# Kernel tuning notes

Measured on AMD Instinct MI355X. Metric: run time of the kernel, lower is better.

The kernel has to match this reference:

```python
import jax, jax.numpy as jnp
import numpy as np

TEMPERATURE = 0.1
MAX_POS = 6
MAX_NEG = 30
POS_NEG_RATIO = 1.0
NEG_K = max(6, MAX_NEG)  # static top-k width for negatives


def setup_inputs() -> dict:
    key = jax.random.key(0)
    k1, k2 = jax.random.split(key)
    K, D = 8192, 256
    features = jax.random.normal(k1, (K, D), dtype=jnp.float32)
    labels = jax.random.randint(k2, (K,), 0, 64, dtype=jnp.int64)
    return {"features": features, "labels": labels}


def reference(features, labels):
    K = features.shape[0]
    # L2-normalize embeddings (F.normalize, dim=1)
    f = features / jnp.clip(jnp.linalg.norm(features, axis=1, keepdims=True), 1e-12)
    sim = jnp.matmul(f, f.T) / TEMPERATURE                      # [K, K]
    sim = sim - jax.lax.stop_gradient(jnp.max(sim, axis=1, keepdims=True))
    exp_sim = jnp.exp(sim)

    eye = jnp.eye(K, dtype=bool)
    same = labels[:, None] == labels[None, :]
    mask_pos = same & ~eye                                      # same label, off-diagonal
    mask_neg = ~same                                            # 1 - mask_pos - eye

    n_pos = jnp.sum(mask_pos, axis=1).astype(jnp.int32)         # [K]
    n_neg = jnp.sum(mask_neg, axis=1).astype(jnp.int32)         # [K]

    # per-anchor dynamic sample counts (vectorized version of the python loop)
    max_pos_i = jnp.minimum(
        n_pos,
        jnp.maximum(1, jnp.minimum(MAX_POS, (n_neg.astype(jnp.float32) * POS_NEG_RATIO).astype(jnp.int32))),
    )
    max_neg_i = jnp.minimum(n_neg, NEG_K)
    valid_row = (n_pos > 0) & (n_neg > 0)
    max_pos_i = jnp.where(valid_row, max_pos_i, 0)
    max_neg_i = jnp.where(valid_row, max_neg_i, 0)

    rows = jnp.arange(K)[:, None]
    neg_inf = jnp.finfo(sim.dtype).min

    # top-k hard positives by similarity, masked to the first max_pos_i ranks
    pos_scores = jnp.where(mask_pos, sim, neg_inf)
    _, pos_idx = jax.lax.top_k(pos_scores, MAX_POS)             # [K, MAX_POS]
    pos_keep = (jnp.arange(MAX_POS)[None, :] < max_pos_i[:, None]).astype(sim.dtype)
    new_mask_pos = jnp.zeros((K, K), sim.dtype).at[rows, pos_idx].add(pos_keep)

    # random negatives: randperm emulated by top-k of uniform scores over neg slots
    rand = jax.random.uniform(jax.random.key(42), (K, K), dtype=jnp.float32)
    neg_scores = jnp.where(mask_neg, rand, -1.0)
    _, neg_idx = jax.lax.top_k(neg_scores, NEG_K)               # [K, NEG_K]
    neg_keep = (jnp.arange(NEG_K)[None, :] < max_neg_i[:, None]).astype(sim.dtype)
    new_mask_neg = jnp.zeros((K, K), sim.dtype).at[rows, neg_idx].add(neg_keep)

    numerator = jnp.sum(exp_sim * new_mask_pos, axis=1)
    denominator = jnp.sum(exp_sim * (new_mask_pos + new_mask_neg), axis=1)
    loss = -jnp.log(jnp.clip(numerator / denominator, 1e-8))
    return jnp.mean(loss)
```

## Files before the change

kernel.cpp:

```cpp
#include <hip/hip_runtime.h>
#include <hip/hip_fp16.h>
#include <math.h>
#include <stdint.h>


#define NEGK 30
#define MAXP 6
#define MAXBC 320
#define RGB 32

typedef _Float16 h2v __attribute__((ext_vector_type(2)));

__device__ __forceinline__ uint64_t mix64(uint64_t z) {
  z += 0x9E3779B97F4A7C15ULL;
  z = (z ^ (z >> 30)) * 0xBF58476D1CE4E5B9ULL;
  z = (z ^ (z >> 27)) * 0x94D049BB133111EBULL;
  return z ^ (z >> 31);
}

__device__ __forceinline__ float wave_reduce_add(float p) {
#pragma unroll
  for (int o = 32; o; o >>= 1) p += __shfl_down(p, o, 64);
  return p;
}

__device__ __forceinline__ float dot8h(uint4 a, uint4 b, float acc) {
  const h2v* pa = (const h2v*)&a;
  const h2v* pb = (const h2v*)&b;
#if __has_builtin(__builtin_amdgcn_fdot2)
#pragma unroll
  for (int q = 0; q < 4; ++q) acc = __builtin_amdgcn_fdot2(pa[q], pb[q], acc, false);
#else
#pragma unroll
  for (int q = 0; q < 4; ++q)
    acc += (float)pa[q].x * (float)pb[q].x + (float)pa[q].y * (float)pb[q].y;
#endif
  return acc;
}

__global__ __launch_bounds__(256) void k_prep(const float* __restrict__ F,
                                              const int* __restrict__ labels, int K,
                                              __half* __restrict__ Fh,
                                              int* __restrict__ g_start,
                                              int* __restrict__ g_soff,
                                              int* __restrict__ g_bucket,
                                              int4* __restrict__ g_meta) {
  __shared__ int cnt[64], start[65], cur[64], soff_s[64];
  const int tid = threadIdx.x;

  if ((int)blockIdx.x < K / 4) {
    const int row = blockIdx.x * 4 + (tid >> 6);
    const int lane = tid & 63;
    const float4 a = ((const float4*)(F + (size_t)row * 256))[lane];
    float p = a.x * a.x + a.y * a.y + a.z * a.z + a.w * a.w;
    p = wave_reduce_add(p);
    p = __shfl(p, 0, 64);
    const float inv = 1.0f / fmaxf(sqrtf(p), 1e-12f);
    union { __half2 h[2]; uint2 u; } cv;
    cv.h[0] = __float22half2_rn(make_float2(a.x * inv, a.y * inv));
    cv.h[1] = __float22half2_rn(make_float2(a.z * inv, a.w * inv));
    ((uint2*)(Fh + (size_t)row * 256))[lane] = cv.u;
    return;
  }

  if (tid < 64) cnt[tid] = 0;
  __syncthreads();
  for (int t = tid; t < K; t += 256) atomicAdd(&cnt[labels[t] & 63], 1);
  __syncthreads();
  if (tid == 0) {
    int acc = 0, sacc = 0;
    for (int l = 0; l < 64; ++l) {
      start[l] = acc;
      const int B = cnt[l];
      acc += B;
      soff_s[l] = sacc;
      const int Bc = B < MAXBC ? B : MAXBC;
      sacc += Bc * Bc;
    }
    start[64] = acc;
  }
  __syncthreads();
  if (tid < 64) { cur[tid] = start[tid]; g_soff[tid] = soff_s[tid]; }
  if (tid < 65) g_start[tid] = start[tid];
  __syncthreads();
  for (int t = tid; t < K; t += 256) {
    const int l = labels[t] & 63;
    const int p = atomicAdd(&cur[l], 1);
    g_bucket[p] = t;
    g_meta[t] = make_int4(start[l], cnt[l], p - start[l], soff_s[l]);
  }
}

template <int NCS>
__device__ __forceinline__ void gram_body(const __half* __restrict__ Fh,
                                          const int* __restrict__ g_bucket,
                                          const uint4* __restrict__ sw,
                                          float* __restrict__ outb,
                                          int bs, int Bc, int r0w, int lane) {
  const uint4* cp[NCS];
  int cq[NCS];
#pragma unroll
  for (int cs = 0; cs < NCS; ++cs) {
    const int cc = cs * 64 + lane;
    const bool valid = (cc < Bc);
    const int gq = g_bucket[bs + (valid ? cc : 0)];
    cq[cs] = valid ? cc : -1;
    cp[cs] = (const uint4*)(Fh + (size_t)gq * 256);
  }

  float acc[8][NCS];
#pragma unroll
  for (int r = 0; r < 8; ++r)
#pragma unroll
    for (int cs = 0; cs < NCS; ++cs) acc[r][cs] = 0.0f;

  for (int k = 0; k < 32; k += 2) {
    uint4 c0[NCS], c1[NCS];
#pragma unroll
    for (int cs = 0; cs < NCS; ++cs) { c0[cs] = cp[cs][k]; c1[cs] = cp[cs][k + 1]; }
#pragma unroll
    for (int r = 0; r < 8; ++r) {
      const uint4 a0 = sw[r * 32 + k];
      const uint4 a1 = sw[r * 32 + k + 1];
#pragma unroll
      for (int cs = 0; cs < NCS; ++cs) {
        acc[r][cs] = dot8h(c0[cs], a0, acc[r][cs]);
        acc[r][cs] = dot8h(c1[cs], a1, acc[r][cs]);
      }
    }
  }

#pragma unroll
  for (int r = 0; r < 8; ++r) {
    const int rr = r0w + r;
    if (rr < Bc) {
#pragma unroll
      for (int cs = 0; cs < NCS; ++cs) {
        const int cc = cq[cs];
        if (cc >= 0)
          outb[(size_t)rr * Bc + cc] = (rr == cc) ? -3.0e38f : acc[r][cs] * 10.0f;
      }
    }
  }
}

__global__ __launch_bounds__(256) void k_gram(const __half* __restrict__ Fh,
                                              const int* __restrict__ g_start,
                                              const int* __restrict__ g_soff,
                                              const int* __restrict__ g_bucket,
                                              float* __restrict__ g_sims) {
  __shared__ uint4 sA[RGB * 32];

  const int b  = blockIdx.x;
  const int bs = g_start[b];
  const int B  = g_start[b + 1] - bs;
  const int Bc = B < MAXBC ? B : MAXBC;
  const int r0 = blockIdx.y * RGB;
  if (r0 >= Bc) return;
  const int tid = threadIdx.x;

  for (int u = tid; u < RGB * 32; u += 256) {
    const int r = u >> 5, c = u & 31;
    const int rr = r0 + r;
    const int gr = g_bucket[bs + (rr < Bc ? rr : 0)];
    sA[u] = ((const uint4*)(Fh + (size_t)gr * 256))[c];
  }
  __syncthreads();

  const int wv = tid >> 6, lane = tid & 63;
  const uint4* sw = sA + (wv * 8) * 32;
  float* outb = g_sims + g_soff[b];
  const int r0w = r0 + wv * 8;

  if (Bc <= 128)
    gram_body<2>(Fh, g_bucket, sw, outb, bs, Bc, r0w, lane);
  else
    gram_body<5>(Fh, g_bucket, sw, outb, bs, Bc, r0w, lane);
}

__global__ __launch_bounds__(256) void k_anchor(
    const __half* __restrict__ Fh, const int* __restrict__ g_bucket,
    const int4* __restrict__ g_meta, const float* __restrict__ g_sims,
    float* __restrict__ g_part, int K) {
  __shared__ uint4 sA[4 * 32];
  const int wv = threadIdx.x >> 6;
  const int lane = threadIdx.x & 63;
  const int i = blockIdx.x * 4 + wv;

  ((uint2*)sA)[wv * 64 + lane] = ((const uint2*)(Fh + (size_t)i * 256))[lane];
  const uint4* sw = sA + wv * 32;

  const int4 mt = g_meta[i];
  const int bs = mt.x, B = mt.y;
  const int Bc = B < MAXBC ? B : MAXBC;
  int loc = mt.z;
  if (loc >= Bc) loc = 0;
  const int n_pos = B - 1;
  const int n_neg = K - B;
  const float* simrow = g_sims + mt.w + (size_t)loc * Bc;

  float v[5];
#pragma unroll
  for (int rr = 0; rr < 5; ++rr) {
    const int t = lane + rr * 64;
    v[rr] = (t < Bc) ? simrow[t] : -3.4e38f;
  }

  int t6 = n_neg < MAXP ? n_neg : MAXP;
  if (t6 < 1) t6 = 1;
  int take = n_pos < t6 ? n_pos : t6;
  if (n_pos <= 0 || n_neg <= 0) take = 0;
  const int target = (take > 0) ? (n_neg < NEGK ? n_neg : NEGK) : 0;

  const int s = lane & 3, g = lane >> 2;
  const int n0 = g, n1 = 16 + g;
  const uint64_t z0 = mix64(((uint64_t)(uint32_t)i << 32) | (uint32_t)n0);
  const uint64_t z1 = mix64(((uint64_t)(uint32_t)i << 32) | (uint32_t)n1);
  const unsigned int r0 = (unsigned int)(((uint64_t)(uint32_t)z0 * (uint64_t)n_neg) >> 32);
  const unsigned int r1 = (unsigned int)(((uint64_t)(uint32_t)z1 * (uint64_t)n_neg) >> 32);
  const int pos0 = (r0 < (unsigned int)bs) ? (int)r0 : (int)r0 + B;
  const int pos1 = (r1 < (unsigned int)bs) ? (int)r1 : (int)r1 + B;
  const bool pv0 = (n0 < target), pv1 = (n1 < target);
  const int j0 = pv0 ? g_bucket[pos0] : 0;
  const int j1 = pv1 ? g_bucket[pos1] : 0;
  const uint4* f0 = (const uint4*)(Fh + (size_t)j0 * 256);
  const uint4* f1 = (const uint4*)(Fh + (size_t)j1 * 256);
  float d0 = 0.0f, d1 = 0.0f;
#pragma unroll
  for (int k = 0; k < 8; ++k) {
    const uint4 aw = sw[k * 4 + s];
    d0 = dot8h(f0[k * 4 + s], aw, d0);
    d1 = dot8h(f1[k * 4 + s], aw, d1);
  }
  d0 += __shfl_xor(d0, 1, 64); d0 += __shfl_xor(d0, 2, 64);
  d1 += __shfl_xor(d1, 1, 64); d1 += __shfl_xor(d1, 2, 64);
  float e = 0.0f;
  if (s == 0) {
    if (pv0) e += expf(d0 * 10.0f);
    if (pv1) e += expf(d1 * 10.0f);
  }
  const float wsum = wave_reduce_add(e);

  float num = 0.0f;
  for (int r = 0; r < take; ++r) {
    float best = v[0];
#pragma unroll
    for (int c = 1; c < 5; ++c) best = fmaxf(best, v[c]);
#pragma unroll
    for (int o = 1; o < 64; o <<= 1) best = fmaxf(best, __shfl_xor(best, o, 64));
    num += expf(best);
#pragma unroll
    for (int c = 0; c < 5; ++c)
      if (v[c] == best) v[c] = -3.4e38f;
  }

  if (lane == 0) {
    float ls = 0.0f;
    if (take > 0) {
      const float denom = num + wsum;
      float ratio = denom > 0.0f ? num / denom : 0.0f;
      ratio = fmaxf(ratio, 1e-8f);
      ls = -logf(ratio);
    }
    g_part[i] = ls;
  }
}

__global__ __launch_bounds__(1024) void k_final(const float* __restrict__ g_part,
                                                float* __restrict__ out, int K) {
  __shared__ float s[16];
  float p = 0.0f;
  for (int t = threadIdx.x; t < K; t += 1024) p += g_part[t];
  p = wave_reduce_add(p);
  if ((threadIdx.x & 63) == 0) s[threadIdx.x >> 6] = p;
  __syncthreads();
  if (threadIdx.x == 0) {
    float tot = 0.0f;
#pragma unroll
    for (int w = 0; w < 16; ++w) tot += s[w];
    out[0] = tot / (float)K;
  }
}

extern "C" void kernel_launch(void* const* d_in, const int* in_sizes, int n_in,
                              void* d_out, int out_size, void* d_ws, size_t ws_size,
                              hipStream_t stream) {
  (void)n_in; (void)out_size; (void)ws_size;
  const float* F = (const float*)d_in[0];
  const int* labels = (const int*)d_in[1];
  const int K = in_sizes[1];
  float* out = (float*)d_out;

  char* ws = (char*)d_ws;
  size_t off = 0;
  int*   g_start  = (int*)(ws + off);   off += 512;
  int*   g_soff   = (int*)(ws + off);   off += 256;
  int*   g_bucket = (int*)(ws + off);   off += (size_t)K * 4;
  float* g_part   = (float*)(ws + off); off += (size_t)K * 4;
  off = (off + 255) & ~(size_t)255;
  int4*  g_meta   = (int4*)(ws + off);  off += (size_t)K * 16;
  __half* Fh      = (__half*)(ws + off); off += (size_t)K * 256 * 2;
  float* g_sims   = (float*)(ws + off);  off += (size_t)MAXBC * K * 4;

  k_prep<<<K / 4 + 1, 256, 0, stream>>>(F, labels, K, Fh, g_start, g_soff,
                                        g_bucket, g_meta);
  {
    dim3 grid(64, (MAXBC + RGB - 1) / RGB, 1);
    k_gram<<<grid, 256, 0, stream>>>(Fh, g_start, g_soff, g_bucket, g_sims);
  }
  k_anchor<<<K / 4, 256, 0, stream>>>(Fh, g_bucket, g_meta, g_sims, g_part, K);
  k_final<<<1, 1024, 0, stream>>>(g_part, out, K);
}
```

Measured before the change: 127.8 us.

## Split gram kernel columns across a third grid dimension of 64-wide tiles

The per-label gram kernel now launches a 3D grid and gives each block one 64-column tile, instead of having each wave loop over up to 5 column slices. This raises the number of blocks and cuts per-thread accumulator registers from 8xNCS to 8, which should improve occupancy and load balance across buckets. In exchange the shared row tile is reloaded once per column tile, and many blocks exit immediately when the bucket is small. Out-of-range row and column indices are now clamped to Bc-1 instead of 0.

New measurement: 114.5 us. -10.4%, faster.

```diff
diff --git a/kernel.cpp b/kernel.cpp
--- a/kernel.cpp
+++ b/kernel.cpp
@@ -8,6 +8,7 @@
 #define MAXP 6
 #define MAXBC 320
 #define RGB 32
+#define CGB 64
 
 typedef _Float16 h2v __attribute__((ext_vector_type(2)));
 
@@ -91,59 +92,6 @@
   }
 }
 
-template <int NCS>
-__device__ __forceinline__ void gram_body(const __half* __restrict__ Fh,
-                                          const int* __restrict__ g_bucket,
-                                          const uint4* __restrict__ sw,
-                                          float* __restrict__ outb,
-                                          int bs, int Bc, int r0w, int lane) {
-  const uint4* cp[NCS];
-  int cq[NCS];
-#pragma unroll
-  for (int cs = 0; cs < NCS; ++cs) {
-    const int cc = cs * 64 + lane;
-    const bool valid = (cc < Bc);
-    const int gq = g_bucket[bs + (valid ? cc : 0)];
-    cq[cs] = valid ? cc : -1;
-    cp[cs] = (const uint4*)(Fh + (size_t)gq * 256);
-  }
-
-  float acc[8][NCS];
-#pragma unroll
-  for (int r = 0; r < 8; ++r)
-#pragma unroll
-    for (int cs = 0; cs < NCS; ++cs) acc[r][cs] = 0.0f;
-
-  for (int k = 0; k < 32; k += 2) {
-    uint4 c0[NCS], c1[NCS];
-#pragma unroll
-    for (int cs = 0; cs < NCS; ++cs) { c0[cs] = cp[cs][k]; c1[cs] = cp[cs][k + 1]; }
-#pragma unroll
-    for (int r = 0; r < 8; ++r) {
-      const uint4 a0 = sw[r * 32 + k];
-      const uint4 a1 = sw[r * 32 + k + 1];
-#pragma unroll
-      for (int cs = 0; cs < NCS; ++cs) {
-        acc[r][cs] = dot8h(c0[cs], a0, acc[r][cs]);
-        acc[r][cs] = dot8h(c1[cs], a1, acc[r][cs]);
-      }
-    }
-  }
-
-#pragma unroll
-  for (int r = 0; r < 8; ++r) {
-    const int rr = r0w + r;
-    if (rr < Bc) {
-#pragma unroll
-      for (int cs = 0; cs < NCS; ++cs) {
-        const int cc = cq[cs];
-        if (cc >= 0)
-          outb[(size_t)rr * Bc + cc] = (rr == cc) ? -3.0e38f : acc[r][cs] * 10.0f;
-      }
-    }
-  }
-}
-
 __global__ __launch_bounds__(256) void k_gram(const __half* __restrict__ Fh,
                                               const int* __restrict__ g_start,
                                               const int* __restrict__ g_soff,
@@ -156,26 +104,50 @@
   const int B  = g_start[b + 1] - bs;
   const int Bc = B < MAXBC ? B : MAXBC;
   const int r0 = blockIdx.y * RGB;
-  if (r0 >= Bc) return;
+  const int c0 = blockIdx.z * CGB;
+  if (r0 >= Bc || c0 >= Bc) return;
   const int tid = threadIdx.x;
 
   for (int u = tid; u < RGB * 32; u += 256) {
     const int r = u >> 5, c = u & 31;
     const int rr = r0 + r;
-    const int gr = g_bucket[bs + (rr < Bc ? rr : 0)];
+    const int gr = g_bucket[bs + (rr < Bc ? rr : Bc - 1)];
     sA[u] = ((const uint4*)(Fh + (size_t)gr * 256))[c];
   }
   __syncthreads();
 
   const int wv = tid >> 6, lane = tid & 63;
-  const uint4* sw = sA + (wv * 8) * 32;
-  float* outb = g_sims + g_soff[b];
-  const int r0w = r0 + wv * 8;
-
-  if (Bc <= 128)
-    gram_body<2>(Fh, g_bucket, sw, outb, bs, Bc, r0w, lane);
-  else
-    gram_body<5>(Fh, g_bucket, sw, outb, bs, Bc, r0w, lane);
+  const int cc = c0 + lane;
+  const int gq = g_bucket[bs + (cc < Bc ? cc : Bc - 1)];
+  const uint4* fq = (const uint4*)(Fh + (size_t)gq * 256);
+  const uint4* sw = sA + wv * 8 * 32;
+
+  float acc[8];
+#pragma unroll
+  for (int r = 0; r < 8; ++r) acc[r] = 0.0f;
+
+  for (int k = 0; k < 32; k += 4) {
+    const uint4 a0 = fq[k], a1 = fq[k + 1], a2 = fq[k + 2], a3 = fq[k + 3];
+#pragma unroll
+    for (int r = 0; r < 8; ++r) {
+      float t = acc[r];
+      t = dot8h(sw[r * 32 + k    ], a0, t);
+      t = dot8h(sw[r * 32 + k + 1], a1, t);
+      t = dot8h(sw[r * 32 + k + 2], a2, t);
+      t = dot8h(sw[r * 32 + k + 3], a3, t);
+      acc[r] = t;
+    }
+  }
+
+  if (cc < Bc) {
+    float* outb = g_sims + g_soff[b];
+#pragma unroll
+    for (int r = 0; r < 8; ++r) {
+      const int rr = r0 + wv * 8 + r;
+      if (rr < Bc)
+        outb[(size_t)rr * Bc + cc] = (rr == cc) ? -3.0e38f : acc[r] * 10.0f;
+    }
+  }
 }
 
 __global__ __launch_bounds__(256) void k_anchor(
@@ -305,7 +277,7 @@
   k_prep<<<K / 4 + 1, 256, 0, stream>>>(F, labels, K, Fh, g_start, g_soff,
                                         g_bucket, g_meta);
   {
-    dim3 grid(64, (MAXBC + RGB - 1) / RGB, 1);
+    dim3 grid(64, (MAXBC + RGB - 1) / RGB, (MAXBC + CGB - 1) / CGB);
     k_gram<<<grid, 256, 0, stream>>>(Fh, g_start, g_soff, g_bucket, g_sims);
   }
   k_anchor<<<K / 4, 256, 0, stream>>>(Fh, g_bucket, g_meta, g_sims, g_part, K);
```
